# Kernel optimization log

Hardware: AMD Instinct MI355X
Metric: run time of the kernel (lower is better)

The kernel has to match this reference:

```python
import jax, jax.numpy as jnp
import numpy as np


def _dct_matrix():
    # orthonormal 8x8 DCT-II matrix, matches cv2.dct
    k = jnp.arange(8.0)[:, None]
    n = jnp.arange(8.0)[None, :]
    D = jnp.sqrt(2.0 / 8.0) * jnp.cos(jnp.pi * (2.0 * n + 1.0) * k / 16.0)
    return D.at[0, :].multiply(1.0 / jnp.sqrt(2.0))


def setup_inputs() -> dict:
    key = jax.random.key(0)
    k = jax.random.split(key, 8)
    C, R = 64, 32  # num_channels, num_channels // reduction_ratio
    return {
        "x": jax.random.uniform(k[0], (256, 256, 3), dtype=jnp.float32),
        "fc1_w": jax.random.normal(k[1], (R, C), dtype=jnp.float32) * 0.1,
        "fc1_b": jax.random.normal(k[2], (R,), dtype=jnp.float32) * 0.1,
        "fc2_w": jax.random.normal(k[3], (C, R), dtype=jnp.float32) * 0.1,
        "fc2_b": jax.random.normal(k[4], (C,), dtype=jnp.float32) * 0.1,
        "sse_w": jax.random.normal(k[5], (C,), dtype=jnp.float32) * 0.1,
        "sse_b": jax.random.normal(k[6], (), dtype=jnp.float32) * 0.1,
        "bs": 64,
    }


def reference(x, fc1_w, fc1_b, fc2_w, fc2_b, sse_w, sse_b, bs):
    D = _dct_matrix().astype(x.dtype)
    # se_dct: channel 0 -> 8x8 blocks (row-major block order) -> per-block 2D DCT
    img = x[:, :, 0]                                           # (256,256)
    blocks = img.reshape(32, 8, 32, 8).transpose(1, 3, 0, 2).reshape(8, 8, 1024)
    dct = jnp.einsum('ik,klc,jl->ijc', D, blocks, D)           # (8,8,1024)
    # se_fre: fre[:,:,i*8+j] = dct[i,j,:].reshape(32,32).T
    fre = dct.reshape(64, 32, 32).transpose(2, 1, 0)           # (32,32,64)
    # ChannelSpatialSELayer on (64,32,32); batch copies are identical so compute once
    feat = fre.transpose(2, 0, 1)                              # (64,32,32)
    sq = feat.mean(axis=(1, 2))                                # (64,)
    h = jax.nn.relu(sq @ fc1_w.T + fc1_b)
    scale_c = jax.nn.sigmoid(h @ fc2_w.T + fc2_b)              # (64,)
    cse = feat * scale_c[:, None, None]
    spatial = jax.nn.sigmoid(jnp.einsum('c,chw->hw', sse_w, feat) + sse_b)
    sse = feat * spatial[None, :, :]
    y = jnp.maximum(cse, sse)                                  # (64,32,32)
    # se_ifre: array[ch//8, ch%8, :] = y_hwc[:,:,ch].T.flatten()
    y_hwc = y.transpose(1, 2, 0)                               # (32,32,64)
    arr = y_hwc.transpose(2, 1, 0).reshape(8, 8, 1024)
    # se_idct: per-block 2D inverse DCT, reassemble 256x256
    idct = jnp.einsum('ki,klc,lj->ijc', D, arr, D)             # (8,8,1024)
    out2d = idct.reshape(8, 8, 32, 32).transpose(2, 0, 3, 1).reshape(256, 256)
    # se_2dto3d + final se_transpose: repeat to 3 channels, tile batch
    return jnp.broadcast_to(out2d[None, None, :, :], (bs, 3, 256, 256))
```

## Files before the change

### kernel.cpp

```cpp
#include <hip/hip_runtime.h>
#include <hip/hip_bf16.h>
#include <math.h>

__device__ __forceinline__ float dctD(int k, int n) {
    const float c[9] = {1.0f, 0.98078528040323043f, 0.92387953251128674f,
                        0.83146961230254524f, 0.70710678118654752f,
                        0.55557023301960218f, 0.38268343236508977f,
                        0.19509032201612825f, 0.0f};
    int m = ((2 * n + 1) * k) & 31;
    float s = 1.0f;
    if (m > 16) m = 32 - m;
    if (m > 8) { m = 16 - m; s = -1.0f; }
    float scale = (k == 0) ? 0.35355339059327373f : 0.5f;
    return scale * s * c[m];
}

__device__ __forceinline__ float sigmoidf(float a) {
    return 1.0f / (1.0f + expf(-a));
}

#define WS_FEAT   0
#define WS_GPART  65536

__global__ __launch_bounds__(256) void dct_kernel(const float* __restrict__ x,
                                                  float* __restrict__ feat,
                                                  float* __restrict__ gpart) {
    __shared__ float Ds[64];
    __shared__ float xs[32][65];
    __shared__ float red[4][64];
    int tid = threadIdx.x;
    if (tid < 64) Ds[tid] = dctD(tid >> 3, tid & 7);
    int b = tid & 31, r = tid >> 5;
    int t = blockIdx.x * 32 + b;
    int br = t >> 5, bc = t & 31;

    const float* xrow = x + ((br * 8 + r) * 256 + bc * 8) * 3;
    float px[8];
    #pragma unroll
    for (int l = 0; l < 8; l++) px[l] = xrow[l * 3];
    #pragma unroll
    for (int l = 0; l < 8; l++) xs[b][r * 8 + l] = px[l];
    __syncthreads();

    float tr[8];
    #pragma unroll
    for (int l = 0; l < 8; l++) tr[l] = 0.f;
    #pragma unroll
    for (int k = 0; k < 8; k++) {
        float d = Ds[r * 8 + k];
        #pragma unroll
        for (int l = 0; l < 8; l++) tr[l] += d * xs[b][k * 8 + l];
    }
    float o[8];
    #pragma unroll
    for (int j = 0; j < 8; j++) {
        float s = 0.f;
        #pragma unroll
        for (int l = 0; l < 8; l++) s += tr[l] * Ds[j * 8 + l];
        o[j] = s;
        feat[(r * 8 + j) * 1024 + t] = s;
    }
    __syncthreads();
    #pragma unroll
    for (int j = 0; j < 8; j++) xs[b][r * 8 + j] = o[j];
    __syncthreads();

    int c = tid & 63, qg = tid >> 6;
    float s = 0.f;
    #pragma unroll
    for (int bb = 0; bb < 8; bb++) s += xs[qg * 8 + bb][c];
    red[qg][c] = s;
    __syncthreads();
    if (tid < 64)
        gpart[blockIdx.x * 64 + tid] =
            red[0][tid] + red[1][tid] + red[2][tid] + red[3][tid];
}

__global__ __launch_bounds__(256) void idct_kernel(const float* __restrict__ feat,
                                                   const float* __restrict__ gpart,
                                                   const float* __restrict__ fc1_w,
                                                   const float* __restrict__ fc1_b,
                                                   const float* __restrict__ fc2_w,
                                                   const float* __restrict__ fc2_b,
                                                   const float* __restrict__ sse_w,
                                                   const float* __restrict__ sse_b,
                                                   float* __restrict__ out0) {
    __shared__ float Ds[64], sw[64], sq[64], sc[64], h[32], spat[32];
    __shared__ float redp[8][33];
    __shared__ float tmls[32][65];
    int tid = threadIdx.x;
    if (tid < 64) {
        Ds[tid] = dctD(tid >> 3, tid & 7);
        sw[tid] = sse_w[tid];
        float s = 0.f;
        #pragma unroll
        for (int w = 0; w < 32; w++) s += gpart[w * 64 + tid];
        sq[tid] = s * (1.0f / 1024.0f);
    }
    __syncthreads();
    if (tid < 32) {
        float a = fc1_b[tid];
        #pragma unroll 8
        for (int cc = 0; cc < 64; cc++) a += sq[cc] * fc1_w[tid * 64 + cc];
        h[tid] = fmaxf(a, 0.f);
    }
    __syncthreads();
    if (tid < 64) {
        float a = fc2_b[tid];
        #pragma unroll 8
        for (int rr = 0; rr < 32; rr++) a += h[rr] * fc2_w[tid * 32 + rr];
        sc[tid] = sigmoidf(a);
    }

    int b = tid & 31, r = tid >> 5;
    int t = blockIdx.x * 32 + b;

    float gr[8];
    #pragma unroll
    for (int l = 0; l < 8; l++) gr[l] = feat[(r * 8 + l) * 1024 + t];
    float sp = 0.f;
    #pragma unroll
    for (int l = 0; l < 8; l++) sp += sw[r * 8 + l] * gr[l];
    redp[r][b] = sp;
    __syncthreads();
    if (tid < 32) {
        float a = sse_b[0];
        #pragma unroll
        for (int rr = 0; rr < 8; rr++) a += redp[rr][tid];
        spat[tid] = sigmoidf(a);
    }
    __syncthreads();

    float spb = spat[b];
    float tm[8];
    #pragma unroll
    for (int j = 0; j < 8; j++) tm[j] = 0.f;
    #pragma unroll
    for (int l = 0; l < 8; l++) {
        float v = gr[l];
        float y = fmaxf(v * sc[r * 8 + l], v * spb);
        #pragma unroll
        for (int j = 0; j < 8; j++) tm[j] += y * Ds[l * 8 + j];
    }
    #pragma unroll
    for (int j = 0; j < 8; j++) tmls[b][r * 8 + j] = tm[j];
    __syncthreads();

    float o[8];
    #pragma unroll
    for (int j = 0; j < 8; j++) o[j] = 0.f;
    #pragma unroll
    for (int k = 0; k < 8; k++) {
        float d = Ds[k * 8 + r];
        #pragma unroll
        for (int j = 0; j < 8; j++) o[j] += d * tmls[b][k * 8 + j];
    }
    int br = t >> 5, bc = t & 31;
    float4* dst = (float4*)(out0 + (br * 8 + r) * 256 + bc * 8);
    dst[0] = make_float4(o[0], o[1], o[2], o[3]);
    dst[1] = make_float4(o[4], o[5], o[6], o[7]);
}

__global__ __launch_bounds__(256) void bcast_kernel(float* __restrict__ out, int total4) {
    const float4* s = (const float4*)out;
    float4* d = (float4*)out;
    int stride = gridDim.x * blockDim.x;
    for (int idx = blockIdx.x * blockDim.x + threadIdx.x + 16384; idx < total4; idx += stride) {
        d[idx] = s[idx & 16383];
    }
}

extern "C" void kernel_launch(void* const* d_in, const int* in_sizes, int n_in,
                              void* d_out, int out_size, void* d_ws, size_t ws_size,
                              hipStream_t stream) {
    const float* x     = (const float*)d_in[0];
    const float* fc1_w = (const float*)d_in[1];
    const float* fc1_b = (const float*)d_in[2];
    const float* fc2_w = (const float*)d_in[3];
    const float* fc2_b = (const float*)d_in[4];
    const float* sse_w = (const float*)d_in[5];
    const float* sse_b = (const float*)d_in[6];
    float* ws = (float*)d_ws;
    float* feat  = ws + WS_FEAT;
    float* gpart = ws + WS_GPART;
    float* out = (float*)d_out;

    dct_kernel<<<32, 256, 0, stream>>>(x, feat, gpart);
    idct_kernel<<<32, 256, 0, stream>>>(feat, gpart, fc1_w, fc1_b, fc2_w, fc2_b,
                                        sse_w, sse_b, out);
    int total4 = out_size / 4;
    bcast_kernel<<<3072, 256, 0, stream>>>(out, total4);
}
```

Baseline: 93.23 us.

## Fuse IDCT with output broadcast and vectorize DCT input loads

Merges the inverse-DCT kernel and the broadcast-copy kernel. 1024 blocks each recompute their 32-block tile, including the small SE MLP, and write it directly to 6 output images from shared memory. This avoids re-reading the first image from global memory and drops one kernel launch, at the cost of redundant DCT/MLP compute per block. The DCT kernel also loads channel-0 pixels with float4 vector loads instead of strided scalar loads.

```diff
diff --git a/kernel.cpp b/kernel.cpp
--- a/kernel.cpp
+++ b/kernel.cpp
@@ -34,12 +34,13 @@
     int t = blockIdx.x * 32 + b;
     int br = t >> 5, bc = t & 31;
 
-    const float* xrow = x + ((br * 8 + r) * 256 + bc * 8) * 3;
-    float px[8];
-    #pragma unroll
-    for (int l = 0; l < 8; l++) px[l] = xrow[l * 3];
-    #pragma unroll
-    for (int l = 0; l < 8; l++) xs[b][r * 8 + l] = px[l];
+    const float4* xrow4 = (const float4*)(x + ((br * 8 + r) * 256 + bc * 8) * 3);
+    float4 v0 = xrow4[0], v1 = xrow4[1], v2 = xrow4[2];
+    float4 v3 = xrow4[3], v4 = xrow4[4], v5 = xrow4[5];
+    xs[b][r * 8 + 0] = v0.x;  xs[b][r * 8 + 1] = v0.w;
+    xs[b][r * 8 + 2] = v1.z;  xs[b][r * 8 + 3] = v2.y;
+    xs[b][r * 8 + 4] = v3.x;  xs[b][r * 8 + 5] = v3.w;
+    xs[b][r * 8 + 6] = v4.z;  xs[b][r * 8 + 7] = v5.y;
     __syncthreads();
 
     float tr[8];
@@ -76,19 +77,24 @@
             red[0][tid] + red[1][tid] + red[2][tid] + red[3][tid];
 }
 
-__global__ __launch_bounds__(256) void idct_kernel(const float* __restrict__ feat,
-                                                   const float* __restrict__ gpart,
-                                                   const float* __restrict__ fc1_w,
-                                                   const float* __restrict__ fc1_b,
-                                                   const float* __restrict__ fc2_w,
-                                                   const float* __restrict__ fc2_b,
-                                                   const float* __restrict__ sse_w,
-                                                   const float* __restrict__ sse_b,
-                                                   float* __restrict__ out0) {
+__global__ __launch_bounds__(256) void idct_bcast_kernel(const float* __restrict__ feat,
+                                                         const float* __restrict__ gpart,
+                                                         const float* __restrict__ fc1_w,
+                                                         const float* __restrict__ fc1_b,
+                                                         const float* __restrict__ fc2_w,
+                                                         const float* __restrict__ fc2_b,
+                                                         const float* __restrict__ sse_w,
+                                                         const float* __restrict__ sse_b,
+                                                         float* __restrict__ out,
+                                                         int nimg) {
     __shared__ float Ds[64], sw[64], sq[64], sc[64], h[32], spat[32];
     __shared__ float redp[8][33];
     __shared__ float tmls[32][65];
+    __shared__ float otile[2048];
     int tid = threadIdx.x;
+    int tg = blockIdx.x & 31;
+    int ig = blockIdx.x >> 5;
+
     if (tid < 64) {
         Ds[tid] = dctD(tid >> 3, tid & 7);
         sw[tid] = sse_w[tid];
@@ -113,7 +119,7 @@
     }
 
     int b = tid & 31, r = tid >> 5;
-    int t = blockIdx.x * 32 + b;
+    int t = tg * 32 + b;
 
     float gr[8];
     #pragma unroll
@@ -155,18 +161,21 @@
         #pragma unroll
         for (int j = 0; j < 8; j++) o[j] += d * tmls[b][k * 8 + j];
     }
-    int br = t >> 5, bc = t & 31;
-    float4* dst = (float4*)(out0 + (br * 8 + r) * 256 + bc * 8);
-    dst[0] = make_float4(o[0], o[1], o[2], o[3]);
-    dst[1] = make_float4(o[4], o[5], o[6], o[7]);
-}
-
-__global__ __launch_bounds__(256) void bcast_kernel(float* __restrict__ out, int total4) {
-    const float4* s = (const float4*)out;
-    float4* d = (float4*)out;
-    int stride = gridDim.x * blockDim.x;
-    for (int idx = blockIdx.x * blockDim.x + threadIdx.x + 16384; idx < total4; idx += stride) {
-        d[idx] = s[idx & 16383];
+    #pragma unroll
+    for (int j = 0; j < 8; j++) otile[r * 256 + b * 8 + j] = o[j];
+    __syncthreads();
+
+    const float4* src = (const float4*)otile;
+    float4 w0 = src[tid];
+    float4 w1 = src[tid + 256];
+    #pragma unroll
+    for (int m = 0; m < 6; m++) {
+        int img = ig * 6 + m;
+        if (img < nimg) {
+            float4* dst = (float4*)(out + (size_t)img * 65536 + tg * 2048);
+            dst[tid] = w0;
+            dst[tid + 256] = w1;
+        }
     }
 }
 
@@ -184,10 +193,10 @@
     float* feat  = ws + WS_FEAT;
     float* gpart = ws + WS_GPART;
     float* out = (float*)d_out;
+    int nimg = out_size / 65536;
 
     dct_kernel<<<32, 256, 0, stream>>>(x, feat, gpart);
-    idct_kernel<<<32, 256, 0, stream>>>(feat, gpart, fc1_w, fc1_b, fc2_w, fc2_b,
-                                        sse_w, sse_b, out);
-    int total4 = out_size / 4;
-    bcast_kernel<<<3072, 256, 0, stream>>>(out, total4);
-}
+    idct_bcast_kernel<<<1024, 256, 0, stream>>>(feat, gpart, fc1_w, fc1_b,
+                                                fc2_w, fc2_b, sse_w, sse_b,
+                                                out, nimg);
+}
```

New measurement: 93.07 us. Within noise of the previous version (-0.2%).
